# Performance work log

Measured on AMD Instinct MI355X. Metric: run time of the kernel, lower is better.

## Reference

```python
import math
import jax, jax.numpy as jnp
import numpy as np

B, NPC, K, D, T, L = 512, 32, 12, 64, 64, 4  # crystals, atoms/crystal, knn, node_dim, time_dim, layers
N = B * NPC
E_IN = 2 * D + 1 + T   # 193
N_IN = 2 * D + T       # 192


def setup_inputs() -> dict:
    key = jax.random.key(0)
    ks = jax.random.split(key, 32)
    rn = lambda k, shp, s=0.05: jax.random.normal(k, shp, jnp.float32) * s
    inp = {}
    inp["z_nodes"] = jax.random.normal(ks[0], (N, 128), jnp.float32)
    inp["t"] = jax.random.uniform(ks[1], (B,), jnp.float32) * 1000.0
    inp["frac_coords"] = jax.random.uniform(ks[2], (N, 3), jnp.float32)
    inp["lattice"] = jnp.eye(3, dtype=jnp.float32) * 5.0 + rn(ks[3], (B, 3, 3), 0.3)
    inp["batch_indices"] = jnp.repeat(jnp.arange(B, dtype=jnp.int32), NPC)
    inp["num_atoms"] = NPC
    # time_mlp: Linear(T, 2T) -> SiLU -> Linear(2T, T)
    inp["time_w1"] = rn(ks[4], (T, 2 * T)); inp["time_b1"] = rn(ks[5], (2 * T,))
    inp["time_w2"] = rn(ks[6], (2 * T, T)); inp["time_b2"] = rn(ks[7], (T,))
    # node_embedding: Linear(128, D)
    inp["emb_w"] = rn(ks[8], (128, D)); inp["emb_b"] = rn(ks[9], (D,))
    # per-layer EGNN params stacked on leading L axis
    inp["edge_w1"] = rn(ks[10], (L, E_IN, D)); inp["edge_b1"] = rn(ks[11], (L, D))
    inp["edge_w2"] = rn(ks[12], (L, D, D));    inp["edge_b2"] = rn(ks[13], (L, D))
    inp["coord_w1"] = rn(ks[14], (L, D, D));   inp["coord_b1"] = rn(ks[15], (L, D))
    inp["coord_w2"] = rn(ks[16], (L, D, 1))
    inp["node_w1"] = rn(ks[17], (L, N_IN, D)); inp["node_b1"] = rn(ks[18], (L, D))
    inp["node_w2"] = rn(ks[19], (L, D, D));    inp["node_b2"] = rn(ks[20], (L, D))
    return inp


def _forward(z_nodes, t, frac_coords, lattice, batch_indices, num_atoms,
             time_w1, time_b1, time_w2, time_b2, emb_w, emb_b,
             edge_w1, edge_b1, edge_w2, edge_b2, coord_w1, coord_b1, coord_w2,
             node_w1, node_b1, node_w2, node_b2):
    silu = jax.nn.silu
    n = num_atoms
    b = lattice.shape[0]
    n_nodes = z_nodes.shape[0]

    # ---- time embedding ----
    half = T // 2
    freqs = jnp.exp(jnp.arange(half, dtype=jnp.float32) * (-math.log(10000.0) / (half - 1)))
    ang = t[:, None] * freqs[None, :]
    sinu = jnp.concatenate([jnp.sin(ang), jnp.cos(ang)], axis=-1)  # [B, T]
    t_feat = silu(sinu @ time_w1 + time_b1) @ time_w2 + time_b2     # [B, T]
    t_nodes = t_feat[batch_indices]                                  # [N, T]

    h = z_nodes @ emb_w + emb_b                                      # [N, D]

    # ---- vectorized PBC KNN graph (all crystals have n atoms) ----
    f = frac_coords.reshape(b, n, 3)
    diff_f = f[:, :, None, :] - f[:, None, :, :]
    diff_f = diff_f - jnp.round(diff_f)
    diff_c = jnp.einsum('bijk,bkl->bijl', diff_f, lattice)           # [b,n,n,3]
    dist_sq = jnp.sum(diff_c * diff_c, axis=-1)                      # [b,n,n]
    dist_sq = jnp.where(jnp.eye(n, dtype=bool)[None], jnp.inf, dist_sq)
    k = min(K, n - 1)
    _, idx = jax.lax.top_k(-dist_sq, k)                              # [b,n,k] neighbor indices
    offs = (jnp.arange(b, dtype=jnp.int32) * n)[:, None, None]
    edge_src = (idx + offs).reshape(-1)                              # neighbors j
    edge_dst = (jnp.broadcast_to(jnp.arange(n, dtype=jnp.int32)[None, :, None], (b, n, k)) + offs).reshape(-1)
    diff_cart = jnp.take_along_axis(diff_c, jnp.broadcast_to(idx[..., None], (b, n, k, 3)), axis=2).reshape(-1, 3)
    dist_sq_e = jnp.take_along_axis(dist_sq, idx, axis=2).reshape(-1, 1)

    t_edges = t_nodes[edge_src]                                      # [E, T]

    total_shift = jnp.zeros((n_nodes, 3), dtype=h.dtype)
    for l in range(L):
        edge_in = jnp.concatenate([h[edge_src], h[edge_dst], dist_sq_e, t_edges], axis=-1)
        m = silu(edge_in @ edge_w1[l] + edge_b1[l])
        m = silu(m @ edge_w2[l] + edge_b2[l])                        # [E, D]
        cw = silu(m @ coord_w1[l] + coord_b1[l]) @ coord_w2[l]       # [E, 1]
        coord_update = jax.ops.segment_sum(diff_cart * cw, edge_src, num_segments=n_nodes)
        m_i = jax.ops.segment_sum(m, edge_dst, num_segments=n_nodes)
        node_in = jnp.concatenate([h, m_i, t_nodes], axis=-1)
        h = h + (silu(node_in @ node_w1[l] + node_b1[l]) @ node_w2[l] + node_b2[l])
        total_shift = total_shift + coord_update

    inv_lat = jnp.linalg.inv(lattice)[batch_indices]                 # [N,3,3]
    shift_frac = jnp.einsum('ni,nij->nj', total_shift, inv_lat)
    return shift_frac, h


def reference(z_nodes, t, frac_coords, lattice, batch_indices, num_atoms,
              time_w1, time_b1, time_w2, time_b2, emb_w, emb_b,
              edge_w1, edge_b1, edge_w2, edge_b2, coord_w1, coord_b1, coord_w2,
              node_w1, node_b1, node_w2, node_b2):
    return _forward(z_nodes, t, frac_coords, lattice, batch_indices, num_atoms,
                    time_w1, time_b1, time_w2, time_b2, emb_w, emb_b,
                    edge_w1, edge_b1, edge_w2, edge_b2, coord_w1, coord_b1, coord_w2,
                    node_w1, node_b1, node_w2, node_b2)
```

## Files before the change

kernel.cpp:

```cpp
#include <hip/hip_runtime.h>
#include <hip/hip_bf16.h>
#include <math.h>

#define NB 512
#define NPC 32
#define KNN 12
#define NL 4
#define NN (NB*NPC)
#define WPL 28672

typedef float v4f __attribute__((ext_vector_type(4)));
typedef float v2f __attribute__((ext_vector_type(2)));
typedef short s8v __attribute__((ext_vector_type(8)));

__device__ __forceinline__ float silu_f(float x) {
    return x * __builtin_amdgcn_rcpf(1.0f + __builtin_amdgcn_exp2f(x * -1.44269504088896341f));
}

__device__ __forceinline__ v2f silu2(v2f x) {
    v2f n = x * -1.44269504088896341f;
    v2f e; e.x = __builtin_amdgcn_exp2f(n.x); e.y = __builtin_amdgcn_exp2f(n.y);
    v2f d = e + 1.0f;
    v2f r; r.x = __builtin_amdgcn_rcpf(d.x); r.y = __builtin_amdgcn_rcpf(d.y);
    return x * r;
}

__device__ __forceinline__ unsigned short f2bf(float x) {
    unsigned u = __float_as_uint(x);
    u += 0x7fffu + ((u >> 16) & 1u);
    return (unsigned short)(u >> 16);
}

__device__ __forceinline__ unsigned pk2bf(float a, float b) {
    __hip_bfloat162 t = __float22bfloat162_rn(make_float2(a, b));
    union { __hip_bfloat162 h; unsigned u; } c; c.h = t;
    return c.u;
}
__device__ __forceinline__ unsigned pk2bfu(v2f s) { return pk2bf(s.x, s.y); }

__device__ __forceinline__ int div12(int e) { return (e * 1366) >> 14; }

template<int R>
__device__ __forceinline__ void gemm_acc(const float* A, int astride,
                                         const float* __restrict__ Wg,
                                         int K, int lane, float* acc) {
#pragma unroll 2
    for (int kq = 0; kq < (K >> 2); ++kq) {
        float w0 = Wg[(4*kq+0)*64 + lane];
        float w1 = Wg[(4*kq+1)*64 + lane];
        float w2 = Wg[(4*kq+2)*64 + lane];
        float w3 = Wg[(4*kq+3)*64 + lane];
#pragma unroll
        for (int r = 0; r < R; ++r) {
            float4 a = *(const float4*)(A + r*astride + 4*kq);
            acc[r] = fmaf(a.x, w0, acc[r]);
            acc[r] = fmaf(a.y, w1, acc[r]);
            acc[r] = fmaf(a.z, w2, acc[r]);
            acc[r] = fmaf(a.w, w3, acc[r]);
        }
    }
}

extern "C" __global__ void prepack_w(const float* __restrict__ edge_w1, const float* __restrict__ edge_w2,
                                     const float* __restrict__ coord_w1, const float* __restrict__ node_w1,
                                     const float* __restrict__ node_w2, unsigned short* __restrict__ wout) {
    int g = blockIdx.x * 256 + threadIdx.x;
    if (g >= 4 * WPL / 8) return;
    int l = (g * 8) / WPL;
    int r = (g * 8) % WPL;
    int base, nKt, mat;
    if      (r < 8192)  { base = 0;     nKt = 2; mat = 0; }
    else if (r < 12288) { base = 8192;  nKt = 2; mat = 1; }
    else if (r < 16384) { base = 12288; nKt = 2; mat = 2; }
    else if (r < 24576) { base = 16384; nKt = 4; mat = 3; }
    else                { base = 24576; nKt = 2; mat = 4; }
    int idx = r - base;
    int lane = (idx >> 3) & 63, t = idx >> 9;
    int kt = t % nKt, nt = t / nKt;
    int k0 = kt*32 + ((lane >> 4) & 3)*8;
    int n  = nt*16 + (lane & 15);
    unsigned short o[8];
#pragma unroll
    for (int j = 0; j < 8; ++j) {
        int k = k0 + j;
        float v;
        if      (mat == 0) v = (n < 64) ? edge_w1[l*193*64 + k*64 + n] : edge_w1[l*193*64 + (64+k)*64 + (n-64)];
        else if (mat == 1) v = edge_w2 [l*4096 + k*64 + n];
        else if (mat == 2) v = coord_w1[l*4096 + k*64 + n];
        else if (mat == 3) v = node_w1 [l*192*64 + k*64 + n];
        else               v = node_w2 [l*4096 + k*64 + n];
        o[j] = f2bf(v);
    }
    *(s8v*)(wout + g*8) = *(s8v*)o;
}

extern "C" __global__ __launch_bounds__(256, 2)
void crystal_fused(const float* __restrict__ z_nodes, const float* __restrict__ t_in,
                   const float* __restrict__ frac,    const float* __restrict__ lattice,
                   const float* __restrict__ time_w1, const float* __restrict__ time_b1,
                   const float* __restrict__ time_w2, const float* __restrict__ time_b2,
                   const float* __restrict__ emb_w,   const float* __restrict__ emb_b,
                   const float* __restrict__ edge_w1, const float* __restrict__ edge_b1,
                   const float* __restrict__ edge_b2, const float* __restrict__ coord_b1,
                   const float* __restrict__ coord_w2,
                   const float* __restrict__ node_w1, const float* __restrict__ node_b1,
                   const float* __restrict__ node_b2,
                   const unsigned short* __restrict__ wbf,
                   float* __restrict__ out)
{
    __shared__ __align__(16) float s_h[32*65];
    __shared__ __align__(16) unsigned short s_habf[32*136];
    __shared__ __align__(16) unsigned short s_n1bf[32*72];
    __shared__ __align__(16) float s_hs[32*68];
    __shared__ __align__(16) float s_hd[32*68];
    __shared__ __align__(16) unsigned short s_tiles16[8192];
    __shared__ float s_dsq[32][33];
    __shared__ float2 s_emeta[384];
    __shared__ float s_endc[384*3];
    __shared__ float s_frac[32][3];
    __shared__ float s_lat[9], s_inv[9];
    __shared__ float s_sinu[64], s_t1[128], s_tf[64];
    __shared__ float s_tb4[NL*64], s_nb4[NL*64];
    __shared__ float s_shift[32*3];

    const int tid  = threadIdx.x;
    const int c    = blockIdx.x;
    const int lane = tid & 63;
    const int wave = tid >> 6;
    const int q4   = lane >> 4;
    const int c16  = lane & 15;
    const int base = c * NPC;

    if (tid < 96) {
        ((float*)s_frac)[tid] = frac[base*3 + tid];
    } else if (tid < 105) {
        s_lat[tid-96] = lattice[c*9 + (tid-96)];
    } else if (tid >= 128 && tid < 160) {
        int i = tid - 128;
        float freq = expf((float)i * (-9.210340371976184f / 31.0f));
        float ang  = t_in[c] * freq;
        s_sinu[i]    = sinf(ang);
        s_sinu[i+32] = cosf(ang);
    }
    __syncthreads();

    float* dcf = (float*)s_tiles16;
    {
        float l00=s_lat[0],l01=s_lat[1],l02=s_lat[2];
        float l10=s_lat[3],l11=s_lat[4],l12=s_lat[5];
        float l20=s_lat[6],l21=s_lat[7],l22=s_lat[8];
        for (int p = tid; p < 1024; p += 256) {
            int i = p >> 5, j = p & 31;
            float dx = s_frac[i][0]-s_frac[j][0];
            float dy = s_frac[i][1]-s_frac[j][1];
            float dz = s_frac[i][2]-s_frac[j][2];
            dx -= rintf(dx); dy -= rintf(dy); dz -= rintf(dz);
            float cx = dx*l00 + dy*l10 + dz*l20;
            float cy = dx*l01 + dy*l11 + dz*l21;
            float cz = dx*l02 + dy*l12 + dz*l22;
            float dd = cx*cx + cy*cy + cz*cz;
            s_dsq[i][j] = (i==j) ? 3.0e38f : dd;
            dcf[p*3+0]=cx; dcf[p*3+1]=cy; dcf[p*3+2]=cz;
        }
    }
    __syncthreads();

    if (tid < 32) {
        int i = tid;
        for (int k = 0; k < KNN; ++k) {
            float best = 3.9e38f; int bj = 0;
            for (int j = 0; j < 32; ++j) {
                float v = s_dsq[i][j];
                if (v < best) { best = v; bj = j; }
            }
            s_dsq[i][bj] = 3.9e38f;
            int e = i*KNN + k;
            s_emeta[e] = make_float2(best, __int_as_float(bj));
            int p = (i<<5) + bj;
            s_endc[e*3+0] = dcf[p*3+0];
            s_endc[e*3+1] = dcf[p*3+1];
            s_endc[e*3+2] = dcf[p*3+2];
        }
    } else if (tid >= 128) {
        int jj = tid - 128;
        float p0 = time_b1[jj], p1=0.f, p2=0.f, p3=0.f;
        for (int k = 0; k < 64; k += 4) {
            p0 = fmaf(s_sinu[k+0], time_w1[(k+0)*128+jj], p0);
            p1 = fmaf(s_sinu[k+1], time_w1[(k+1)*128+jj], p1);
            p2 = fmaf(s_sinu[k+2], time_w1[(k+2)*128+jj], p2);
            p3 = fmaf(s_sinu[k+3], time_w1[(k+3)*128+jj], p3);
        }
        s_t1[jj] = silu_f((p0+p1) + (p2+p3));
    }
    __syncthreads();

    if (tid < 64) {
        float p0=time_b2[tid],p1=0.f,p2=0.f,p3=0.f;
        for (int k = 0; k < 128; k += 4) {
            p0 = fmaf(s_t1[k+0], time_w2[(k+0)*64+tid], p0);
            p1 = fmaf(s_t1[k+1], time_w2[(k+1)*64+tid], p1);
            p2 = fmaf(s_t1[k+2], time_w2[(k+2)*64+tid], p2);
            p3 = fmaf(s_t1[k+3], time_w2[(k+3)*64+tid], p3);
        }
        s_tf[tid] = (p0+p1) + (p2+p3);
    } else if (tid < 160) {
        s_shift[tid-64] = 0.0f;
    }
    __syncthreads();

    float* zbuf = (float*)s_tiles16;
    for (int q = tid; q < 4096; q += 256) zbuf[q] = z_nodes[base*128 + q];
#pragma unroll
    for (int it = 0; it < 2; ++it) {
        int t = wave + it*4;
        int lt = t >> 1, kind = t & 1;
        const float* Wt = kind ? (node_w1 + lt*192*64 + 128*64) : (edge_w1 + lt*193*64 + 129*64);
        const float* bb = kind ? (node_b1 + lt*64) : (edge_b1 + lt*64);
        float p0 = bb[lane], p1=0.f, p2=0.f, p3=0.f;
        for (int k = 0; k < 64; k += 4) {
            p0 = fmaf(s_tf[k+0], Wt[(k+0)*64 + lane], p0);
            p1 = fmaf(s_tf[k+1], Wt[(k+1)*64 + lane], p1);
            p2 = fmaf(s_tf[k+2], Wt[(k+2)*64 + lane], p2);
            p3 = fmaf(s_tf[k+3], Wt[(k+3)*64 + lane], p3);
        }
        float v = (p0+p1) + (p2+p3);
        if (kind) s_nb4[lt*64 + lane] = v;
        else      s_tb4[lt*64 + lane] = v;
    }
    __syncthreads();

    {
        float acc[8];
#pragma unroll
        for (int r = 0; r < 8; ++r) acc[r] = emb_b[lane];
        gemm_acc<8>(zbuf + (wave*8)*128, 128, emb_w, 128, lane, acc);
#pragma unroll
        for (int r = 0; r < 8; ++r) {
            int row = wave*8 + r;
            s_h[row*65 + lane] = acc[r];
            s_habf[row*136 + lane] = f2bf(acc[r]);
        }
    }
    __syncthreads();

    for (int l = 0; l < NL; ++l) {
        const unsigned short* wl = wbf + l*WPL;
        const float* w1row = edge_w1 + l*193*64 + 128*64;
        float b2e_v[4], cb1_v[4], w2c_v[4];
#pragma unroll
        for (int nt = 0; nt < 4; ++nt) {
            b2e_v[nt] = edge_b2 [l*64 + nt*16 + c16];
            cb1_v[nt] = coord_b1[l*64 + nt*16 + c16];
            w2c_v[nt] = coord_w2[l*64 + nt*16 + c16];
        }

        s8v w2f[8], wc1f[8];
#pragma unroll
        for (int nt = 0; nt < 4; ++nt)
#pragma unroll
            for (int kt = 0; kt < 2; ++kt) {
                w2f [nt*2+kt] = *(const s8v*)(wl +  8192 + ((nt*2+kt)*64 + lane)*8);
                wc1f[nt*2+kt] = *(const s8v*)(wl + 12288 + ((nt*2+kt)*64 + lane)*8);
            }
        union F4 { float4 v; float f[4]; };
        F4 W4[4];
        W4[0].v = *(const float4*)(w1row + q4*8);
        W4[1].v = *(const float4*)(w1row + q4*8 + 4);
        W4[2].v = *(const float4*)(w1row + 32 + q4*8);
        W4[3].v = *(const float4*)(w1row + 32 + q4*8 + 4);

        {
            s8v a[2][2];
#pragma unroll
            for (int mt = 0; mt < 2; ++mt)
#pragma unroll
                for (int kt = 0; kt < 2; ++kt)
                    a[mt][kt] = *(const s8v*)(s_habf + (mt*16 + c16)*136 + kt*32 + q4*8);
            v4f accS[2] = {{0.f,0.f,0.f,0.f},{0.f,0.f,0.f,0.f}};
            v4f accD[2] = {{0.f,0.f,0.f,0.f},{0.f,0.f,0.f,0.f}};
#pragma unroll
            for (int kt = 0; kt < 2; ++kt) {
                s8v bS = *(const s8v*)(wl + ((wave*2+kt)*64 + lane)*8);
                s8v bD = *(const s8v*)(wl + (((wave+4)*2+kt)*64 + lane)*8);
#pragma unroll
                for (int mt = 0; mt < 2; ++mt) {
                    accS[mt] = __builtin_amdgcn_mfma_f32_16x16x32_bf16(a[mt][kt], bS, accS[mt], 0, 0, 0);
                    accD[mt] = __builtin_amdgcn_mfma_f32_16x16x32_bf16(a[mt][kt], bD, accD[mt], 0, 0, 0);
                }
            }
            int col = wave*16 + c16;
            float tbv = s_tb4[l*64 + col];
#pragma unroll
            for (int mt = 0; mt < 2; ++mt)
#pragma unroll
                for (int reg = 0; reg < 4; ++reg) {
                    int row = mt*16 + q4*4 + reg;
                    s_hs[row*68 + col] = accS[mt][reg];
                    s_hd[row*68 + col] = accD[mt][reg] + tbv;
                }
        }
        __syncthreads();

        {
            unsigned short* tile = s_tiles16 + wave*1152;
            float miacc[4][2];
#pragma unroll
            for (int a2 = 0; a2 < 4; ++a2) { miacc[a2][0] = 0.f; miacc[a2][1] = 0.f; }

            auto flushd = [&](int d) {
                int s = d & 1;
#pragma unroll
                for (int nt = 0; nt < 4; ++nt) {
                    float v = miacc[nt][s];
                    v += __shfl_xor(v, 16);
                    v += __shfl_xor(v, 32);
                    s_habf[(wave*8 + d)*136 + 64 + nt*16 + c16] = f2bf(v);
                    miacc[nt][s] = 0.f;
                }
            };

            float2 me0 = s_emeta[wave*96 +  0 + c16];
            float2 me1 = s_emeta[wave*96 + 16 + c16];
            float2 me2 = s_emeta[wave*96 + 32 + c16];
            float2 me3 = s_emeta[wave*96 + 48 + c16];
            float2 me4 = s_emeta[wave*96 + 64 + c16];
            float2 me5 = s_emeta[wave*96 + 80 + c16];

            F4 H[4], G[4];
            {
                int srcn = __float_as_int(me0.y);
                int dstn = div12(wave*96 + c16);
                const float* hsr = s_hs + srcn*68 + q4*8;
                const float* hdr = s_hd + dstn*68 + q4*8;
                H[0].v = *(const float4*)(hsr);      H[1].v = *(const float4*)(hsr+4);
                H[2].v = *(const float4*)(hsr+32);   H[3].v = *(const float4*)(hsr+36);
                G[0].v = *(const float4*)(hdr);      G[1].v = *(const float4*)(hdr+4);
                G[2].v = *(const float4*)(hdr+32);   G[3].v = *(const float4*)(hdr+36);
            }

#pragma unroll
            for (int m = 0; m < 6; ++m) {
                const int e0g = wave*96 + m*16;
                const float dq = (m==0) ? me0.x : (m==1) ? me1.x : (m==2) ? me2.x
                               : (m==3) ? me3.x : (m==4) ? me4.x : me5.x;
                union S8 { s8v v; unsigned u[4]; } A0, A1;
#pragma unroll
                for (int g2 = 0; g2 < 4; ++g2) {
                    v2f h0 = {H[g2].f[0], H[g2].f[1]}, h1 = {H[g2].f[2], H[g2].f[3]};
                    v2f g0 = {G[g2].f[0], G[g2].f[1]}, g1 = {G[g2].f[2], G[g2].f[3]};
                    v2f w0 = {W4[g2].f[0], W4[g2].f[1]}, w1 = {W4[g2].f[2], W4[g2].f[3]};
                    v2f t0 = h0 + g0 + w0 * dq;
                    v2f t1 = h1 + g1 + w1 * dq;
                    unsigned lo  = pk2bfu(silu2(t0));
                    unsigned hi2 = pk2bfu(silu2(t1));
                    if (g2 < 2) { A0.u[g2*2] = lo; A0.u[g2*2+1] = hi2; }
                    else        { A1.u[(g2-2)*2] = lo; A1.u[(g2-2)*2+1] = hi2; }
                }
                if (m < 5) {
                    float2 men = (m==0) ? me1 : (m==1) ? me2 : (m==2) ? me3
                               : (m==3) ? me4 : me5;
                    int srcn = __float_as_int(men.y);
                    int dstn = div12(e0g + 16 + c16);
                    const float* hsr = s_hs + srcn*68 + q4*8;
                    const float* hdr = s_hd + dstn*68 + q4*8;
                    H[0].v = *(const float4*)(hsr);      H[1].v = *(const float4*)(hsr+4);
                    H[2].v = *(const float4*)(hsr+32);   H[3].v = *(const float4*)(hsr+36);
                    G[0].v = *(const float4*)(hdr);      G[1].v = *(const float4*)(hdr+4);
                    G[2].v = *(const float4*)(hdr+32);   G[3].v = *(const float4*)(hdr+36);
                }

                const int dlo = (m < 3) ? m : m + 1;
                const int thr = 3 - (m % 3);
                const int slo = dlo & 1;
#pragma unroll
                for (int nt = 0; nt < 4; ++nt) {
                    v4f acc = {0.f,0.f,0.f,0.f};
                    acc = __builtin_amdgcn_mfma_f32_16x16x32_bf16(A0.v, w2f[nt*2+0], acc, 0,0,0);
                    acc = __builtin_amdgcn_mfma_f32_16x16x32_bf16(A1.v, w2f[nt*2+1], acc, 0,0,0);
                    int col = nt*16 + c16;
                    v2f z01 = {acc[0] + b2e_v[nt], acc[1] + b2e_v[nt]};
                    v2f z23 = {acc[2] + b2e_v[nt], acc[3] + b2e_v[nt]};
                    v2f s01 = silu2(z01), s23 = silu2(z23);
                    unsigned p01 = pk2bfu(s01), p23 = pk2bfu(s23);
                    tile[(q4*4 + 0)*72 + col] = (unsigned short)p01;
                    tile[(q4*4 + 1)*72 + col] = (unsigned short)(p01 >> 16);
                    tile[(q4*4 + 2)*72 + col] = (unsigned short)p23;
                    tile[(q4*4 + 3)*72 + col] = (unsigned short)(p23 >> 16);
                    float msum = (s01.x + s01.y) + (s23.x + s23.y);
                    bool hi = (q4 >= thr);
                    miacc[nt][slo]     += hi ? 0.f : msum;
                    miacc[nt][slo ^ 1] += hi ? msum : 0.f;
                }
                asm volatile("s_waitcnt lgkmcnt(0)" ::: "memory");
                s8v c0 = *(const s8v*)(tile + c16*72 +      q4*8);
                s8v c1 = *(const s8v*)(tile + c16*72 + 32 + q4*8);
                v2f cwp01 = {0.f, 0.f}, cwp23 = {0.f, 0.f};
#pragma unroll
                for (int nt = 0; nt < 4; ++nt) {
                    v4f acc = {0.f,0.f,0.f,0.f};
                    acc = __builtin_amdgcn_mfma_f32_16x16x32_bf16(c0, wc1f[nt*2+0], acc, 0,0,0);
                    acc = __builtin_amdgcn_mfma_f32_16x16x32_bf16(c1, wc1f[nt*2+1], acc, 0,0,0);
                    v2f z01 = {acc[0] + cb1_v[nt], acc[1] + cb1_v[nt]};
                    v2f z23 = {acc[2] + cb1_v[nt], acc[3] + cb1_v[nt]};
                    cwp01 += silu2(z01) * w2c_v[nt];
                    cwp23 += silu2(z23) * w2c_v[nt];
                }
                float cwp[4] = {cwp01.x, cwp01.y, cwp23.x, cwp23.y};
#pragma unroll
                for (int reg = 0; reg < 4; ++reg) {
                    float v = cwp[reg];
                    v += __shfl_xor(v, 1); v += __shfl_xor(v, 2);
                    v += __shfl_xor(v, 4); v += __shfl_xor(v, 8);
                    int e = e0g + q4*4 + reg;
                    if (c16 < 3) {
                        int src = __float_as_int(s_emeta[e].y);
                        atomicAdd(&s_shift[src*3 + c16], s_endc[e*3 + c16] * v);
                    }
                }
                if (m == 0) { flushd(0); }
                else if (m == 1) { flushd(1); }
                else if (m == 2) { flushd(2); flushd(3); }
                else if (m == 3) { flushd(4); }
                else if (m == 4) { flushd(5); }
                else             { flushd(6); flushd(7); }
            }
        }

        const int mtA = wave & 1, nt0 = wave >> 1, nt1 = (wave >> 1) + 2;
        s8v bn1[8];
#pragma unroll
        for (int kt = 0; kt < 4; ++kt) {
            bn1[kt]   = *(const s8v*)(wl + 16384 + ((nt0*4+kt)*64 + lane)*8);
            bn1[4+kt] = *(const s8v*)(wl + 16384 + ((nt1*4+kt)*64 + lane)*8);
        }
        __syncthreads();

        {
            s8v aA[4];
#pragma unroll
            for (int kt = 0; kt < 4; ++kt)
                aA[kt] = *(const s8v*)(s_habf + (mtA*16 + c16)*136 + kt*32 + q4*8);
#pragma unroll
            for (int it = 0; it < 2; ++it) {
                int nt = it ? nt1 : nt0;
                int col = nt*16 + c16;
                float nbc = s_nb4[l*64 + col];
                v4f acc = {0.f,0.f,0.f,0.f};
#pragma unroll
                for (int kt = 0; kt < 4; ++kt)
                    acc = __builtin_amdgcn_mfma_f32_16x16x32_bf16(aA[kt], bn1[it*4+kt], acc, 0,0,0);
                v2f z01 = {acc[0] + nbc, acc[1] + nbc};
                v2f z23 = {acc[2] + nbc, acc[3] + nbc};
                unsigned p01 = pk2bfu(silu2(z01)), p23 = pk2bfu(silu2(z23));
                int r0 = mtA*16 + q4*4;
                s_n1bf[(r0+0)*72 + col] = (unsigned short)p01;
                s_n1bf[(r0+1)*72 + col] = (unsigned short)(p01 >> 16);
                s_n1bf[(r0+2)*72 + col] = (unsigned short)p23;
                s_n1bf[(r0+3)*72 + col] = (unsigned short)(p23 >> 16);
            }
        }
        s8v bn2[4];
        bn2[0] = *(const s8v*)(wl + 24576 + ((nt0*2+0)*64 + lane)*8);
        bn2[1] = *(const s8v*)(wl + 24576 + ((nt0*2+1)*64 + lane)*8);
        bn2[2] = *(const s8v*)(wl + 24576 + ((nt1*2+0)*64 + lane)*8);
        bn2[3] = *(const s8v*)(wl + 24576 + ((nt1*2+1)*64 + lane)*8);
        __syncthreads();

        {
            s8v a0 = *(const s8v*)(s_n1bf + (mtA*16 + c16)*72 +      q4*8);
            s8v a1 = *(const s8v*)(s_n1bf + (mtA*16 + c16)*72 + 32 + q4*8);
#pragma unroll
            for (int it = 0; it < 2; ++it) {
                int nt = it ? nt1 : nt0;
                int col = nt*16 + c16;
                float nb2_v = node_b2[l*64 + col];
                v4f acc = {0.f,0.f,0.f,0.f};
                acc = __builtin_amdgcn_mfma_f32_16x16x32_bf16(a0, bn2[it*2+0], acc, 0,0,0);
                acc = __builtin_amdgcn_mfma_f32_16x16x32_bf16(a1, bn2[it*2+1], acc, 0,0,0);
#pragma unroll
                for (int reg = 0; reg < 4; ++reg) {
                    int row = mtA*16 + q4*4 + reg;
                    float hn = s_h[row*65 + col] + acc[reg] + nb2_v;
                    s_h[row*65 + col] = hn;
                    s_habf[row*136 + col] = f2bf(hn);
                }
            }
        }
        __syncthreads();
    }

    if (tid == 0) {
        float a=s_lat[0],b=s_lat[1],cc=s_lat[2];
        float d=s_lat[3],e=s_lat[4],f =s_lat[5];
        float g=s_lat[6],h2=s_lat[7],i2=s_lat[8];
        float A  =  (e*i2 - f*h2);
        float Bm = -(d*i2 - f*g);
        float C  =  (d*h2 - e*g);
        float det = a*A + b*Bm + cc*C;
        float rd = 1.0f/det;
        s_inv[0] = A*rd;
        s_inv[1] = -(b*i2 - cc*h2)*rd;
        s_inv[2] =  (b*f  - cc*e )*rd;
        s_inv[3] = Bm*rd;
        s_inv[4] =  (a*i2 - cc*g )*rd;
        s_inv[5] = -(a*f  - cc*d )*rd;
        s_inv[6] = C*rd;
        s_inv[7] = -(a*h2 - b*g  )*rd;
        s_inv[8] =  (a*e  - b*d  )*rd;
    }
    __syncthreads();
    if (tid < 96) {
        int r = tid/3, j = tid%3;
        float v = s_shift[r*3+0]*s_inv[0*3+j]
                + s_shift[r*3+1]*s_inv[1*3+j]
                + s_shift[r*3+2]*s_inv[2*3+j];
        out[(base + r)*3 + j] = v;
    }
    for (int q = tid; q < 2048; q += 256) {
        int row = q >> 6, colq = q & 63;
        out[NN*3 + base*64 + q] = s_h[row*65 + colq];
    }
}

extern "C" void kernel_launch(void* const* d_in, const int* in_sizes, int n_in,
                              void* d_out, int out_size, void* d_ws, size_t ws_size,
                              hipStream_t stream) {
    unsigned short* wbf = (unsigned short*)d_ws;
    prepack_w<<<(4*WPL/8 + 255)/256, 256, 0, stream>>>(
        (const float*)d_in[12], (const float*)d_in[14], (const float*)d_in[16],
        (const float*)d_in[19], (const float*)d_in[21], wbf);
    crystal_fused<<<NB, 256, 0, stream>>>(
        (const float*)d_in[0],  (const float*)d_in[1],  (const float*)d_in[2],  (const float*)d_in[3],
        (const float*)d_in[6],  (const float*)d_in[7],  (const float*)d_in[8],  (const float*)d_in[9],
        (const float*)d_in[10], (const float*)d_in[11],
        (const float*)d_in[12], (const float*)d_in[13], (const float*)d_in[15],
        (const float*)d_in[17], (const float*)d_in[18],
        (const float*)d_in[19], (const float*)d_in[20], (const float*)d_in[22],
        wbf, (float*)d_out);
}
```

Measured before the change: 196.5 us.

## Double block to 512 threads and repartition per-wave work across eight waves

Each crystal's block grows from 4 to 8 waves. Every phase is re-split so each wave handles half as much: edge message rows, node MLP tiles, and the src/dst projection are now separate waves. KNN selection becomes 8 lanes per atom with shuffle-based argmin reduction, and the node embedding reads z directly from global memory instead of staging it in LDS. This aims to raise parallelism and cut serial per-block latency, at the cost of more registers and LDS per block, lower occupancy headroom, and a larger shared tile.

```diff
diff --git a/kernel.cpp b/kernel.cpp
--- a/kernel.cpp
+++ b/kernel.cpp
@@ -94,7 +94,7 @@
     *(s8v*)(wout + g*8) = *(s8v*)o;
 }
 
-extern "C" __global__ __launch_bounds__(256, 2)
+extern "C" __global__ __launch_bounds__(512, 4)
 void crystal_fused(const float* __restrict__ z_nodes, const float* __restrict__ t_in,
                    const float* __restrict__ frac,    const float* __restrict__ lattice,
                    const float* __restrict__ time_w1, const float* __restrict__ time_b1,
@@ -113,7 +113,7 @@
     __shared__ __align__(16) unsigned short s_n1bf[32*72];
     __shared__ __align__(16) float s_hs[32*68];
     __shared__ __align__(16) float s_hd[32*68];
-    __shared__ __align__(16) unsigned short s_tiles16[8192];
+    __shared__ __align__(16) unsigned short s_tiles16[9216];
     __shared__ float s_dsq[32][33];
     __shared__ float2 s_emeta[384];
     __shared__ float s_endc[384*3];
@@ -149,7 +149,7 @@
         float l00=s_lat[0],l01=s_lat[1],l02=s_lat[2];
         float l10=s_lat[3],l11=s_lat[4],l12=s_lat[5];
         float l20=s_lat[6],l21=s_lat[7],l22=s_lat[8];
-        for (int p = tid; p < 1024; p += 256) {
+        for (int p = tid; p < 1024; p += 512) {
             int i = p >> 5, j = p & 31;
             float dx = s_frac[i][0]-s_frac[j][0];
             float dy = s_frac[i][1]-s_frac[j][1];
@@ -165,24 +165,42 @@
     }
     __syncthreads();
 
-    if (tid < 32) {
-        int i = tid;
+    if (tid < 256) {
+        int i = tid >> 3, g = tid & 7;
+        float d0 = s_dsq[i][g*4+0];
+        float d1 = s_dsq[i][g*4+1];
+        float d2 = s_dsq[i][g*4+2];
+        float d3 = s_dsq[i][g*4+3];
         for (int k = 0; k < KNN; ++k) {
-            float best = 3.9e38f; int bj = 0;
-            for (int j = 0; j < 32; ++j) {
-                float v = s_dsq[i][j];
-                if (v < best) { best = v; bj = j; }
-            }
-            s_dsq[i][bj] = 3.9e38f;
-            int e = i*KNN + k;
-            s_emeta[e] = make_float2(best, __int_as_float(bj));
-            int p = (i<<5) + bj;
-            s_endc[e*3+0] = dcf[p*3+0];
-            s_endc[e*3+1] = dcf[p*3+1];
-            s_endc[e*3+2] = dcf[p*3+2];
-        }
-    } else if (tid >= 128) {
-        int jj = tid - 128;
+            float v = d0; int jl = g*4;
+            if (d1 < v) { v = d1; jl = g*4+1; }
+            if (d2 < v) { v = d2; jl = g*4+2; }
+            if (d3 < v) { v = d3; jl = g*4+3; }
+            float ov; int oj;
+            ov = __shfl_xor(v, 1); oj = __shfl_xor(jl, 1);
+            if (ov < v || (ov == v && oj < jl)) { v = ov; jl = oj; }
+            ov = __shfl_xor(v, 2); oj = __shfl_xor(jl, 2);
+            if (ov < v || (ov == v && oj < jl)) { v = ov; jl = oj; }
+            ov = __shfl_xor(v, 4); oj = __shfl_xor(jl, 4);
+            if (ov < v || (ov == v && oj < jl)) { v = ov; jl = oj; }
+            if ((jl >> 2) == g) {
+                int s = jl & 3;
+                if      (s == 0) d0 = 3.9e38f;
+                else if (s == 1) d1 = 3.9e38f;
+                else if (s == 2) d2 = 3.9e38f;
+                else             d3 = 3.9e38f;
+            }
+            if (g == 0) {
+                int e = i*KNN + k;
+                s_emeta[e] = make_float2(v, __int_as_float(jl));
+                int p = (i<<5) + jl;
+                s_endc[e*3+0] = dcf[p*3+0];
+                s_endc[e*3+1] = dcf[p*3+1];
+                s_endc[e*3+2] = dcf[p*3+2];
+            }
+        }
+    } else if (tid < 384) {
+        int jj = tid - 256;
         float p0 = time_b1[jj], p1=0.f, p2=0.f, p3=0.f;
         for (int k = 0; k < 64; k += 4) {
             p0 = fmaf(s_sinu[k+0], time_w1[(k+0)*128+jj], p0);
@@ -208,12 +226,8 @@
     }
     __syncthreads();
 
-    float* zbuf = (float*)s_tiles16;
-    for (int q = tid; q < 4096; q += 256) zbuf[q] = z_nodes[base*128 + q];
-#pragma unroll
-    for (int it = 0; it < 2; ++it) {
-        int t = wave + it*4;
-        int lt = t >> 1, kind = t & 1;
+    {
+        int lt = wave >> 1, kind = wave & 1;
         const float* Wt = kind ? (node_w1 + lt*192*64 + 128*64) : (edge_w1 + lt*193*64 + 129*64);
         const float* bb = kind ? (node_b1 + lt*64) : (edge_b1 + lt*64);
         float p0 = bb[lane], p1=0.f, p2=0.f, p3=0.f;
@@ -227,16 +241,14 @@
         if (kind) s_nb4[lt*64 + lane] = v;
         else      s_tb4[lt*64 + lane] = v;
     }
-    __syncthreads();
-
     {
-        float acc[8];
-#pragma unroll
-        for (int r = 0; r < 8; ++r) acc[r] = emb_b[lane];
-        gemm_acc<8>(zbuf + (wave*8)*128, 128, emb_w, 128, lane, acc);
-#pragma unroll
-        for (int r = 0; r < 8; ++r) {
-            int row = wave*8 + r;
+        float acc[4];
+#pragma unroll
+        for (int r = 0; r < 4; ++r) acc[r] = emb_b[lane];
+        gemm_acc<4>(z_nodes + (base + wave*4)*128, 128, emb_w, 128, lane, acc);
+#pragma unroll
+        for (int r = 0; r < 4; ++r) {
+            int row = wave*4 + r;
             s_h[row*65 + lane] = acc[r];
             s_habf[row*136 + lane] = f2bf(acc[r]);
         }
@@ -270,34 +282,36 @@
         W4[3].v = *(const float4*)(w1row + 32 + q4*8 + 4);
 
         {
+            const int wn = wave & 3;
             s8v a[2][2];
 #pragma unroll
             for (int mt = 0; mt < 2; ++mt)
 #pragma unroll
                 for (int kt = 0; kt < 2; ++kt)
                     a[mt][kt] = *(const s8v*)(s_habf + (mt*16 + c16)*136 + kt*32 + q4*8);
-            v4f accS[2] = {{0.f,0.f,0.f,0.f},{0.f,0.f,0.f,0.f}};
-            v4f accD[2] = {{0.f,0.f,0.f,0.f},{0.f,0.f,0.f,0.f}};
+            v4f acc[2] = {{0.f,0.f,0.f,0.f},{0.f,0.f,0.f,0.f}};
 #pragma unroll
             for (int kt = 0; kt < 2; ++kt) {
-                s8v bS = *(const s8v*)(wl + ((wave*2+kt)*64 + lane)*8);
-                s8v bD = *(const s8v*)(wl + (((wave+4)*2+kt)*64 + lane)*8);
-#pragma unroll
-                for (int mt = 0; mt < 2; ++mt) {
-                    accS[mt] = __builtin_amdgcn_mfma_f32_16x16x32_bf16(a[mt][kt], bS, accS[mt], 0, 0, 0);
-                    accD[mt] = __builtin_amdgcn_mfma_f32_16x16x32_bf16(a[mt][kt], bD, accD[mt], 0, 0, 0);
-                }
-            }
-            int col = wave*16 + c16;
-            float tbv = s_tb4[l*64 + col];
-#pragma unroll
-            for (int mt = 0; mt < 2; ++mt)
-#pragma unroll
-                for (int reg = 0; reg < 4; ++reg) {
-                    int row = mt*16 + q4*4 + reg;
-                    s_hs[row*68 + col] = accS[mt][reg];
-                    s_hd[row*68 + col] = accD[mt][reg] + tbv;
-                }
+                s8v b = *(const s8v*)(wl + (((wn + (wave >= 4 ? 4 : 0))*2 + kt)*64 + lane)*8);
+#pragma unroll
+                for (int mt = 0; mt < 2; ++mt)
+                    acc[mt] = __builtin_amdgcn_mfma_f32_16x16x32_bf16(a[mt][kt], b, acc[mt], 0, 0, 0);
+            }
+            int col = wn*16 + c16;
+            if (wave >= 4) {
+                float tbv = s_tb4[l*64 + col];
+#pragma unroll
+                for (int mt = 0; mt < 2; ++mt)
+#pragma unroll
+                    for (int reg = 0; reg < 4; ++reg)
+                        s_hd[(mt*16 + q4*4 + reg)*68 + col] = acc[mt][reg] + tbv;
+            } else {
+#pragma unroll
+                for (int mt = 0; mt < 2; ++mt)
+#pragma unroll
+                    for (int reg = 0; reg < 4; ++reg)
+                        s_hs[(mt*16 + q4*4 + reg)*68 + col] = acc[mt][reg];
+            }
         }
         __syncthreads();
 
@@ -314,22 +328,19 @@
                     float v = miacc[nt][s];
                     v += __shfl_xor(v, 16);
                     v += __shfl_xor(v, 32);
-                    s_habf[(wave*8 + d)*136 + 64 + nt*16 + c16] = f2bf(v);
+                    s_habf[(wave*4 + d)*136 + 64 + nt*16 + c16] = f2bf(v);
                     miacc[nt][s] = 0.f;
                 }
             };
 
-            float2 me0 = s_emeta[wave*96 +  0 + c16];
-            float2 me1 = s_emeta[wave*96 + 16 + c16];
-            float2 me2 = s_emeta[wave*96 + 32 + c16];
-            float2 me3 = s_emeta[wave*96 + 48 + c16];
-            float2 me4 = s_emeta[wave*96 + 64 + c16];
-            float2 me5 = s_emeta[wave*96 + 80 + c16];
+            float2 me0 = s_emeta[wave*48 +  0 + c16];
+            float2 me1 = s_emeta[wave*48 + 16 + c16];
+            float2 me2 = s_emeta[wave*48 + 32 + c16];
 
             F4 H[4], G[4];
             {
                 int srcn = __float_as_int(me0.y);
-                int dstn = div12(wave*96 + c16);
+                int dstn = div12(wave*48 + c16);
                 const float* hsr = s_hs + srcn*68 + q4*8;
                 const float* hdr = s_hd + dstn*68 + q4*8;
                 H[0].v = *(const float4*)(hsr);      H[1].v = *(const float4*)(hsr+4);
@@ -339,10 +350,9 @@
             }
 
 #pragma unroll
-            for (int m = 0; m < 6; ++m) {
-                const int e0g = wave*96 + m*16;
-                const float dq = (m==0) ? me0.x : (m==1) ? me1.x : (m==2) ? me2.x
-                               : (m==3) ? me3.x : (m==4) ? me4.x : me5.x;
+            for (int m = 0; m < 3; ++m) {
+                const int e0g = wave*48 + m*16;
+                const float dq = (m==0) ? me0.x : (m==1) ? me1.x : me2.x;
                 union S8 { s8v v; unsigned u[4]; } A0, A1;
 #pragma unroll
                 for (int g2 = 0; g2 < 4; ++g2) {
@@ -356,9 +366,8 @@
                     if (g2 < 2) { A0.u[g2*2] = lo; A0.u[g2*2+1] = hi2; }
                     else        { A1.u[(g2-2)*2] = lo; A1.u[(g2-2)*2+1] = hi2; }
                 }
-                if (m < 5) {
-                    float2 men = (m==0) ? me1 : (m==1) ? me2 : (m==2) ? me3
-                               : (m==3) ? me4 : me5;
+                if (m < 2) {
+                    float2 men = (m==0) ? me1 : me2;
                     int srcn = __float_as_int(men.y);
                     int dstn = div12(e0g + 16 + c16);
                     const float* hsr = s_hs + srcn*68 + q4*8;
@@ -369,9 +378,8 @@
                     G[2].v = *(const float4*)(hdr+32);   G[3].v = *(const float4*)(hdr+36);
                 }
 
-                const int dlo = (m < 3) ? m : m + 1;
-                const int thr = 3 - (m % 3);
-                const int slo = dlo & 1;
+                const int thr = 3 - m;
+                const int slo = m & 1;
 #pragma unroll
                 for (int nt = 0; nt < 4; ++nt) {
                     v4f acc = {0.f,0.f,0.f,0.f};
@@ -417,22 +425,17 @@
                         atomicAdd(&s_shift[src*3 + c16], s_endc[e*3 + c16] * v);
                     }
                 }
-                if (m == 0) { flushd(0); }
+                if (m == 0)      { flushd(0); }
                 else if (m == 1) { flushd(1); }
-                else if (m == 2) { flushd(2); flushd(3); }
-                else if (m == 3) { flushd(4); }
-                else if (m == 4) { flushd(5); }
-                else             { flushd(6); flushd(7); }
-            }
-        }
-
-        const int mtA = wave & 1, nt0 = wave >> 1, nt1 = (wave >> 1) + 2;
-        s8v bn1[8];
-#pragma unroll
-        for (int kt = 0; kt < 4; ++kt) {
-            bn1[kt]   = *(const s8v*)(wl + 16384 + ((nt0*4+kt)*64 + lane)*8);
-            bn1[4+kt] = *(const s8v*)(wl + 16384 + ((nt1*4+kt)*64 + lane)*8);
-        }
+                else             { flushd(2); flushd(3); }
+            }
+        }
+
+        const int mtA = wave & 1, ntA = wave >> 1;
+        s8v bn1[4];
+#pragma unroll
+        for (int kt = 0; kt < 4; ++kt)
+            bn1[kt] = *(const s8v*)(wl + 16384 + ((ntA*4+kt)*64 + lane)*8);
         __syncthreads();
 
         {
@@ -440,50 +443,40 @@
 #pragma unroll
             for (int kt = 0; kt < 4; ++kt)
                 aA[kt] = *(const s8v*)(s_habf + (mtA*16 + c16)*136 + kt*32 + q4*8);
-#pragma unroll
-            for (int it = 0; it < 2; ++it) {
-                int nt = it ? nt1 : nt0;
-                int col = nt*16 + c16;
-                float nbc = s_nb4[l*64 + col];
-                v4f acc = {0.f,0.f,0.f,0.f};
-#pragma unroll
-                for (int kt = 0; kt < 4; ++kt)
-                    acc = __builtin_amdgcn_mfma_f32_16x16x32_bf16(aA[kt], bn1[it*4+kt], acc, 0,0,0);
-                v2f z01 = {acc[0] + nbc, acc[1] + nbc};
-                v2f z23 = {acc[2] + nbc, acc[3] + nbc};
-                unsigned p01 = pk2bfu(silu2(z01)), p23 = pk2bfu(silu2(z23));
-                int r0 = mtA*16 + q4*4;
-                s_n1bf[(r0+0)*72 + col] = (unsigned short)p01;
-                s_n1bf[(r0+1)*72 + col] = (unsigned short)(p01 >> 16);
-                s_n1bf[(r0+2)*72 + col] = (unsigned short)p23;
-                s_n1bf[(r0+3)*72 + col] = (unsigned short)(p23 >> 16);
-            }
-        }
-        s8v bn2[4];
-        bn2[0] = *(const s8v*)(wl + 24576 + ((nt0*2+0)*64 + lane)*8);
-        bn2[1] = *(const s8v*)(wl + 24576 + ((nt0*2+1)*64 + lane)*8);
-        bn2[2] = *(const s8v*)(wl + 24576 + ((nt1*2+0)*64 + lane)*8);
-        bn2[3] = *(const s8v*)(wl + 24576 + ((nt1*2+1)*64 + lane)*8);
+            int col = ntA*16 + c16;
+            float nbc = s_nb4[l*64 + col];
+            v4f acc = {0.f,0.f,0.f,0.f};
+#pragma unroll
+            for (int kt = 0; kt < 4; ++kt)
+                acc = __builtin_amdgcn_mfma_f32_16x16x32_bf16(aA[kt], bn1[kt], acc, 0,0,0);
+            v2f z01 = {acc[0] + nbc, acc[1] + nbc};
+            v2f z23 = {acc[2] + nbc, acc[3] + nbc};
+            unsigned p01 = pk2bfu(silu2(z01)), p23 = pk2bfu(silu2(z23));
+            int r0 = mtA*16 + q4*4;
+            s_n1bf[(r0+0)*72 + col] = (unsigned short)p01;
+            s_n1bf[(r0+1)*72 + col] = (unsigned short)(p01 >> 16);
+            s_n1bf[(r0+2)*72 + col] = (unsigned short)p23;
+            s_n1bf[(r0+3)*72 + col] = (unsigned short)(p23 >> 16);
+        }
+        s8v bn2[2];
+        bn2[0] = *(const s8v*)(wl + 24576 + ((ntA*2+0)*64 + lane)*8);
+        bn2[1] = *(const s8v*)(wl + 24576 + ((ntA*2+1)*64 + lane)*8);
         __syncthreads();
 
         {
             s8v a0 = *(const s8v*)(s_n1bf + (mtA*16 + c16)*72 +      q4*8);
             s8v a1 = *(const s8v*)(s_n1bf + (mtA*16 + c16)*72 + 32 + q4*8);
-#pragma unroll
-            for (int it = 0; it < 2; ++it) {
-                int nt = it ? nt1 : nt0;
-                int col = nt*16 + c16;
-                float nb2_v = node_b2[l*64 + col];
-                v4f acc = {0.f,0.f,0.f,0.f};
-                acc = __builtin_amdgcn_mfma_f32_16x16x32_bf16(a0, bn2[it*2+0], acc, 0,0,0);
-                acc = __builtin_amdgcn_mfma_f32_16x16x32_bf16(a1, bn2[it*2+1], acc, 0,0,0);
-#pragma unroll
-                for (int reg = 0; reg < 4; ++reg) {
-                    int row = mtA*16 + q4*4 + reg;
-                    float hn = s_h[row*65 + col] + acc[reg] + nb2_v;
-                    s_h[row*65 + col] = hn;
-                    s_habf[row*136 + col] = f2bf(hn);
-                }
+            int col = ntA*16 + c16;
+            float nb2_v = node_b2[l*64 + col];
+            v4f acc = {0.f,0.f,0.f,0.f};
+            acc = __builtin_amdgcn_mfma_f32_16x16x32_bf16(a0, bn2[0], acc, 0,0,0);
+            acc = __builtin_amdgcn_mfma_f32_16x16x32_bf16(a1, bn2[1], acc, 0,0,0);
+#pragma unroll
+            for (int reg = 0; reg < 4; ++reg) {
+                int row = mtA*16 + q4*4 + reg;
+                float hn = s_h[row*65 + col] + acc[reg] + nb2_v;
+                s_h[row*65 + col] = hn;
+                s_habf[row*136 + col] = f2bf(hn);
             }
         }
         __syncthreads();
@@ -516,7 +509,7 @@
                 + s_shift[r*3+2]*s_inv[2*3+j];
         out[(base + r)*3 + j] = v;
     }
-    for (int q = tid; q < 2048; q += 256) {
+    for (int q = tid; q < 2048; q += 512) {
         int row = q >> 6, colq = q & 63;
         out[NN*3 + base*64 + q] = s_h[row*65 + colq];
     }
@@ -529,7 +522,7 @@
     prepack_w<<<(4*WPL/8 + 255)/256, 256, 0, stream>>>(
         (const float*)d_in[12], (const float*)d_in[14], (const float*)d_in[16],
         (const float*)d_in[19], (const float*)d_in[21], wbf);
-    crystal_fused<<<NB, 256, 0, stream>>>(
+    crystal_fused<<<NB, 512, 0, stream>>>(
         (const float*)d_in[0],  (const float*)d_in[1],  (const float*)d_in[2],  (const float*)d_in[3],
         (const float*)d_in[6],  (const float*)d_in[7],  (const float*)d_in[8],  (const float*)d_in[9],
         (const float*)d_in[10], (const float*)d_in[11],
```

After: 372.0 us. 89.3% more time.

## Parallelize kNN selection, double-buffer edge tiles, per-wave shift accumulators

Applied to the files above, without the earlier changes.

kNN top-12 selection now uses four threads per atom, each holding eight distances in registers and combining its local minimum through cross-lane shuffles, instead of one thread scanning all 32 candidates. The per-wave edge tile is double-buffered across m-iterations, and computing the next edge activations moves after the current MFMAs to overlap LDS latency. Coordinate-shift atomics now go to per-wave copies that are summed at the end, which removes contention between waves. The edge_w1 time row is staged in shared memory and the distance scratch reuses an existing LDS buffer. This costs more LDS for tiles and extra registers.

```diff
diff --git a/kernel.cpp b/kernel.cpp
--- a/kernel.cpp
+++ b/kernel.cpp
@@ -113,15 +113,19 @@
     __shared__ __align__(16) unsigned short s_n1bf[32*72];
     __shared__ __align__(16) float s_hs[32*68];
     __shared__ __align__(16) float s_hd[32*68];
-    __shared__ __align__(16) unsigned short s_tiles16[8192];
-    __shared__ float s_dsq[32][33];
+    __shared__ __align__(16) unsigned short s_tiles16[9216];
     __shared__ float2 s_emeta[384];
     __shared__ float s_endc[384*3];
     __shared__ float s_frac[32][3];
     __shared__ float s_lat[9], s_inv[9];
     __shared__ float s_sinu[64], s_t1[128], s_tf[64];
     __shared__ float s_tb4[NL*64], s_nb4[NL*64];
-    __shared__ float s_shift[32*3];
+    __shared__ float s_shift4[4*96];
+    __shared__ float s_shift[96];
+    __shared__ float s_w1r[64];
+
+    float* dcf = (float*)s_tiles16;
+    float (*s_dsq)[33] = (float(*)[33])s_n1bf;
 
     const int tid  = threadIdx.x;
     const int c    = blockIdx.x;
@@ -144,7 +148,6 @@
     }
     __syncthreads();
 
-    float* dcf = (float*)s_tiles16;
     {
         float l00=s_lat[0],l01=s_lat[1],l02=s_lat[2];
         float l10=s_lat[3],l11=s_lat[4],l12=s_lat[5];
@@ -165,23 +168,47 @@
     }
     __syncthreads();
 
-    if (tid < 32) {
-        int i = tid;
+    if (tid < 128) {
+        int i = tid >> 2, g = tid & 3;
+        float dl0 = s_dsq[i][g*8+0], dl1 = s_dsq[i][g*8+1];
+        float dl2 = s_dsq[i][g*8+2], dl3 = s_dsq[i][g*8+3];
+        float dl4 = s_dsq[i][g*8+4], dl5 = s_dsq[i][g*8+5];
+        float dl6 = s_dsq[i][g*8+6], dl7 = s_dsq[i][g*8+7];
         for (int k = 0; k < KNN; ++k) {
-            float best = 3.9e38f; int bj = 0;
-            for (int j = 0; j < 32; ++j) {
-                float v = s_dsq[i][j];
-                if (v < best) { best = v; bj = j; }
-            }
-            s_dsq[i][bj] = 3.9e38f;
-            int e = i*KNN + k;
-            s_emeta[e] = make_float2(best, __int_as_float(bj));
-            int p = (i<<5) + bj;
-            s_endc[e*3+0] = dcf[p*3+0];
-            s_endc[e*3+1] = dcf[p*3+1];
-            s_endc[e*3+2] = dcf[p*3+2];
-        }
-    } else if (tid >= 128) {
+            float v = dl0; int jl = g*8;
+            if (dl1 < v) { v = dl1; jl = g*8+1; }
+            if (dl2 < v) { v = dl2; jl = g*8+2; }
+            if (dl3 < v) { v = dl3; jl = g*8+3; }
+            if (dl4 < v) { v = dl4; jl = g*8+4; }
+            if (dl5 < v) { v = dl5; jl = g*8+5; }
+            if (dl6 < v) { v = dl6; jl = g*8+6; }
+            if (dl7 < v) { v = dl7; jl = g*8+7; }
+            float ov; int oj;
+            ov = __shfl_xor(v, 1); oj = __shfl_xor(jl, 1);
+            if (ov < v || (ov == v && oj < jl)) { v = ov; jl = oj; }
+            ov = __shfl_xor(v, 2); oj = __shfl_xor(jl, 2);
+            if (ov < v || (ov == v && oj < jl)) { v = ov; jl = oj; }
+            if ((jl >> 3) == g) {
+                int s = jl & 7;
+                if      (s == 0) dl0 = 3.9e38f;
+                else if (s == 1) dl1 = 3.9e38f;
+                else if (s == 2) dl2 = 3.9e38f;
+                else if (s == 3) dl3 = 3.9e38f;
+                else if (s == 4) dl4 = 3.9e38f;
+                else if (s == 5) dl5 = 3.9e38f;
+                else if (s == 6) dl6 = 3.9e38f;
+                else             dl7 = 3.9e38f;
+            }
+            if (g == 0) {
+                int e = i*KNN + k;
+                s_emeta[e] = make_float2(v, __int_as_float(jl));
+                int p = (i<<5) + jl;
+                s_endc[e*3+0] = dcf[p*3+0];
+                s_endc[e*3+1] = dcf[p*3+1];
+                s_endc[e*3+2] = dcf[p*3+2];
+            }
+        }
+    } else {
         int jj = tid - 128;
         float p0 = time_b1[jj], p1=0.f, p2=0.f, p3=0.f;
         for (int k = 0; k < 64; k += 4) {
@@ -203,8 +230,8 @@
             p3 = fmaf(s_t1[k+3], time_w2[(k+3)*64+tid], p3);
         }
         s_tf[tid] = (p0+p1) + (p2+p3);
-    } else if (tid < 160) {
-        s_shift[tid-64] = 0.0f;
+    } else {
+        for (int q = tid - 64; q < 384; q += 192) s_shift4[q] = 0.0f;
     }
     __syncthreads();
 
@@ -245,7 +272,9 @@
 
     for (int l = 0; l < NL; ++l) {
         const unsigned short* wl = wbf + l*WPL;
-        const float* w1row = edge_w1 + l*193*64 + 128*64;
+
+        if (tid < 64) s_w1r[tid] = edge_w1[l*193*64 + 128*64 + tid];
+
         float b2e_v[4], cb1_v[4], w2c_v[4];
 #pragma unroll
         for (int nt = 0; nt < 4; ++nt) {
@@ -262,12 +291,6 @@
                 w2f [nt*2+kt] = *(const s8v*)(wl +  8192 + ((nt*2+kt)*64 + lane)*8);
                 wc1f[nt*2+kt] = *(const s8v*)(wl + 12288 + ((nt*2+kt)*64 + lane)*8);
             }
-        union F4 { float4 v; float f[4]; };
-        F4 W4[4];
-        W4[0].v = *(const float4*)(w1row + q4*8);
-        W4[1].v = *(const float4*)(w1row + q4*8 + 4);
-        W4[2].v = *(const float4*)(w1row + 32 + q4*8);
-        W4[3].v = *(const float4*)(w1row + 32 + q4*8 + 4);
 
         {
             s8v a[2][2];
@@ -302,7 +325,8 @@
         __syncthreads();
 
         {
-            unsigned short* tile = s_tiles16 + wave*1152;
+            unsigned short* tbase = s_tiles16 + wave*2304;
+            float* myshift = s_shift4 + wave*96;
             float miacc[4][2];
 #pragma unroll
             for (int a2 = 0; a2 < 4; ++a2) { miacc[a2][0] = 0.f; miacc[a2][1] = 0.f; }
@@ -326,48 +350,32 @@
             float2 me4 = s_emeta[wave*96 + 64 + c16];
             float2 me5 = s_emeta[wave*96 + 80 + c16];
 
-            F4 H[4], G[4];
+            union S8 { s8v v; unsigned u[4]; } A0, A1;
             {
                 int srcn = __float_as_int(me0.y);
                 int dstn = div12(wave*96 + c16);
-                const float* hsr = s_hs + srcn*68 + q4*8;
-                const float* hdr = s_hd + dstn*68 + q4*8;
-                H[0].v = *(const float4*)(hsr);      H[1].v = *(const float4*)(hsr+4);
-                H[2].v = *(const float4*)(hsr+32);   H[3].v = *(const float4*)(hsr+36);
-                G[0].v = *(const float4*)(hdr);      G[1].v = *(const float4*)(hdr+4);
-                G[2].v = *(const float4*)(hdr+32);   G[3].v = *(const float4*)(hdr+36);
-            }
-
-#pragma unroll
-            for (int m = 0; m < 6; ++m) {
-                const int e0g = wave*96 + m*16;
-                const float dq = (m==0) ? me0.x : (m==1) ? me1.x : (m==2) ? me2.x
-                               : (m==3) ? me3.x : (m==4) ? me4.x : me5.x;
-                union S8 { s8v v; unsigned u[4]; } A0, A1;
+                const float* hsr = s_hs + srcn*68;
+                const float* hdr = s_hd + dstn*68;
+                const float dq = me0.x;
 #pragma unroll
                 for (int g2 = 0; g2 < 4; ++g2) {
-                    v2f h0 = {H[g2].f[0], H[g2].f[1]}, h1 = {H[g2].f[2], H[g2].f[3]};
-                    v2f g0 = {G[g2].f[0], G[g2].f[1]}, g1 = {G[g2].f[2], G[g2].f[3]};
-                    v2f w0 = {W4[g2].f[0], W4[g2].f[1]}, w1 = {W4[g2].f[2], W4[g2].f[3]};
-                    v2f t0 = h0 + g0 + w0 * dq;
-                    v2f t1 = h1 + g1 + w1 * dq;
+                    int off = ((g2 & 2) ? 32 : 0) + ((g2 & 1) ? 4 : 0) + q4*8;
+                    float4 Hv = *(const float4*)(hsr + off);
+                    float4 Gv = *(const float4*)(hdr + off);
+                    float4 Wv = *(const float4*)(s_w1r + off);
+                    v2f t0 = {Hv.x + Gv.x + Wv.x*dq, Hv.y + Gv.y + Wv.y*dq};
+                    v2f t1 = {Hv.z + Gv.z + Wv.z*dq, Hv.w + Gv.w + Wv.w*dq};
                     unsigned lo  = pk2bfu(silu2(t0));
                     unsigned hi2 = pk2bfu(silu2(t1));
                     if (g2 < 2) { A0.u[g2*2] = lo; A0.u[g2*2+1] = hi2; }
                     else        { A1.u[(g2-2)*2] = lo; A1.u[(g2-2)*2+1] = hi2; }
                 }
-                if (m < 5) {
-                    float2 men = (m==0) ? me1 : (m==1) ? me2 : (m==2) ? me3
-                               : (m==3) ? me4 : me5;
-                    int srcn = __float_as_int(men.y);
-                    int dstn = div12(e0g + 16 + c16);
-                    const float* hsr = s_hs + srcn*68 + q4*8;
-                    const float* hdr = s_hd + dstn*68 + q4*8;
-                    H[0].v = *(const float4*)(hsr);      H[1].v = *(const float4*)(hsr+4);
-                    H[2].v = *(const float4*)(hsr+32);   H[3].v = *(const float4*)(hsr+36);
-                    G[0].v = *(const float4*)(hdr);      G[1].v = *(const float4*)(hdr+4);
-                    G[2].v = *(const float4*)(hdr+32);   G[3].v = *(const float4*)(hdr+36);
-                }
+            }
+
+#pragma unroll
+            for (int m = 0; m < 6; ++m) {
+                const int e0g = wave*96 + m*16;
+                unsigned short* tile = tbase + (m & 1)*1152;
 
                 const int dlo = (m < 3) ? m : m + 1;
                 const int thr = 3 - (m % 3);
@@ -391,6 +399,30 @@
                     miacc[nt][slo]     += hi ? 0.f : msum;
                     miacc[nt][slo ^ 1] += hi ? msum : 0.f;
                 }
+
+                if (m < 5) {
+                    float2 men = (m==0) ? me1 : (m==1) ? me2 : (m==2) ? me3
+                               : (m==3) ? me4 : me5;
+                    int srcn = __float_as_int(men.y);
+                    int dstn = div12(e0g + 16 + c16);
+                    const float* hsr = s_hs + srcn*68;
+                    const float* hdr = s_hd + dstn*68;
+                    const float dqn = men.x;
+#pragma unroll
+                    for (int g2 = 0; g2 < 4; ++g2) {
+                        int off = ((g2 & 2) ? 32 : 0) + ((g2 & 1) ? 4 : 0) + q4*8;
+                        float4 Hv = *(const float4*)(hsr + off);
+                        float4 Gv = *(const float4*)(hdr + off);
+                        float4 Wv = *(const float4*)(s_w1r + off);
+                        v2f t0 = {Hv.x + Gv.x + Wv.x*dqn, Hv.y + Gv.y + Wv.y*dqn};
+                        v2f t1 = {Hv.z + Gv.z + Wv.z*dqn, Hv.w + Gv.w + Wv.w*dqn};
+                        unsigned lo  = pk2bfu(silu2(t0));
+                        unsigned hi2 = pk2bfu(silu2(t1));
+                        if (g2 < 2) { A0.u[g2*2] = lo; A0.u[g2*2+1] = hi2; }
+                        else        { A1.u[(g2-2)*2] = lo; A1.u[(g2-2)*2+1] = hi2; }
+                    }
+                }
+
                 asm volatile("s_waitcnt lgkmcnt(0)" ::: "memory");
                 s8v c0 = *(const s8v*)(tile + c16*72 +      q4*8);
                 s8v c1 = *(const s8v*)(tile + c16*72 + 32 + q4*8);
@@ -414,7 +446,7 @@
                     int e = e0g + q4*4 + reg;
                     if (c16 < 3) {
                         int src = __float_as_int(s_emeta[e].y);
-                        atomicAdd(&s_shift[src*3 + c16], s_endc[e*3 + c16] * v);
+                        atomicAdd(&myshift[src*3 + c16], s_endc[e*3 + c16] * v);
                     }
                 }
                 if (m == 0) { flushd(0); }
@@ -508,6 +540,10 @@
         s_inv[7] = -(a*h2 - b*g  )*rd;
         s_inv[8] =  (a*e  - b*d  )*rd;
     }
+    if (tid < 96) {
+        s_shift[tid] = s_shift4[tid] + s_shift4[96 + tid]
+                     + s_shift4[192 + tid] + s_shift4[288 + tid];
+    }
     __syncthreads();
     if (tid < 96) {
         int r = tid/3, j = tid%3;
```

Measured after the change: 204.4 us. 4.0% more time.
